# Kernel tuning notes

Measured on AMD Instinct MI355X. Metric: run time of the kernel, lower is better.

The kernel has to match this reference:

```python
import jax, jax.numpy as jnp
import numpy as np

LN_EPS = 1e-6
IGNORE_INDEX = -100

D_MODEL = 768
VOCAB = 32128
B, S = 4, 512


def setup_inputs() -> dict:
    key = jax.random.key(0)
    k1, k2, k3 = jax.random.split(key, 3)
    hidden_states = jax.random.normal(k1, (B, S, D_MODEL), dtype=jnp.float32)
    labels = jax.random.randint(k2, (B, S), 0, VOCAB, dtype=jnp.int64)
    ln_weight = jnp.ones((D_MODEL,), dtype=jnp.float32)
    # nn.Linear(d_model, vocab, bias=False).weight has shape [vocab, d_model]
    lm_head_weight = jax.random.normal(k3, (VOCAB, D_MODEL), dtype=jnp.float32) * (D_MODEL ** -0.5)
    return {
        "hidden_states": hidden_states,
        "labels": labels,
        "ln_weight": ln_weight,
        "lm_head_weight": lm_head_weight,
    }


def t5_layer_norm(x, weight, eps=LN_EPS):
    # T5-style RMSNorm: no mean subtraction, variance in fp32
    variance = jnp.mean(x.astype(jnp.float32) ** 2, axis=-1, keepdims=True)
    x = x * jax.lax.rsqrt(variance + eps)
    return weight * x


def reference(hidden_states, labels, ln_weight, lm_head_weight):
    h = t5_layer_norm(hidden_states, ln_weight)
    # dropout is identity in eval / rate=0
    # lm_head: [B,S,D] @ [V,D]^T -> [B,S,V]
    prediction_scores = jnp.einsum("bsd,vd->bsv", h, lm_head_weight)
    # CrossEntropyLoss(ignore_index=-100), mean over non-ignored tokens
    logits = prediction_scores.reshape(-1, VOCAB)  # [B*S, V]
    flat_labels = labels.reshape(-1)
    valid = flat_labels != IGNORE_INDEX
    safe_labels = jnp.where(valid, flat_labels, 0)
    logp = jax.nn.log_softmax(logits, axis=-1)
    nll = -jnp.take_along_axis(logp, safe_labels[:, None], axis=-1)[:, 0]
    nll = jnp.where(valid, nll, 0.0)
    loss = jnp.sum(nll) / jnp.maximum(jnp.sum(valid.astype(jnp.float32)), 1.0)
    return (loss, prediction_scores)
```

## Files before the change

kernel.cpp:

```cpp
#include <hip/hip_runtime.h>
#include <stdint.h>

#define DM 768
#define VOC 32128
#define NTOK 2048
#define IGN (-100)

typedef __bf16 bf16x8 __attribute__((ext_vector_type(8)));
typedef float f32x4 __attribute__((ext_vector_type(4)));

typedef __attribute__((address_space(1))) void gvoid_t;
typedef __attribute__((address_space(3))) void svoid_t;

__device__ __forceinline__ void gl_lds16(const void* g, void* s) {
  __builtin_amdgcn_global_load_lds((gvoid_t*)g, (svoid_t*)s, 16, 0, 0);
}

__device__ __forceinline__ unsigned short f2bf(float f) {
  unsigned int u = __float_as_uint(f);
  u = (u + 0x7fffu + ((u >> 16) & 1u)) >> 16;
  return (unsigned short)u;
}

__global__ void __launch_bounds__(256) cvt_w_kernel(const float* __restrict__ W,
                                                    unsigned short* __restrict__ Wb) {
  size_t i = ((size_t)blockIdx.x * 256 + threadIdx.x) * 4;
  float4 v = *(const float4*)(W + i);
  ushort4 o;
  o.x = f2bf(v.x); o.y = f2bf(v.y); o.z = f2bf(v.z); o.w = f2bf(v.w);
  *(ushort4*)(Wb + i) = o;
}

__global__ void __launch_bounds__(256) rmsnorm_kernel(const float* __restrict__ x,
                                                      const float* __restrict__ w,
                                                      unsigned short* __restrict__ h) {
  int tok = blockIdx.x;
  const float* xr = x + (size_t)tok * DM;
  int t = threadIdx.x;
  float v0 = xr[t], v1 = xr[t + 256], v2 = xr[t + 512];
  float ss = v0 * v0 + v1 * v1 + v2 * v2;
  for (int off = 32; off; off >>= 1) ss += __shfl_down(ss, off);
  __shared__ float red[4];
  int wv = t >> 6, ln = t & 63;
  if (ln == 0) red[wv] = ss;
  __syncthreads();
  float tot = red[0] + red[1] + red[2] + red[3];
  float inv = rsqrtf(tot * (1.0f / DM) + 1e-6f);
  unsigned short* hr = h + (size_t)tok * DM;
  hr[t]       = f2bf(v0 * inv * w[t]);
  hr[t + 256] = f2bf(v1 * inv * w[t + 256]);
  hr[t + 512] = f2bf(v2 * inv * w[t + 512]);
}

__global__ void __launch_bounds__(256, 2) gemm_kernel(const unsigned short* __restrict__ A,
                                                      const unsigned short* __restrict__ Bw,
                                                      float* __restrict__ C) {
  __shared__ __align__(16) unsigned short As[128 * 32];
  __shared__ __align__(16) unsigned short Bs[128 * 32];

  const int m0 = blockIdx.x * 128;
  const int n0 = blockIdx.y * 128;
  const int tid = threadIdx.x;
  const int wv = tid >> 6, ln = tid & 63;
  const int srow = ln >> 2;
  const int scol = (ln & 3) * 8;

  const unsigned short* aSrc0 = A + (size_t)(m0 + wv * 32 + srow) * DM + scol;
  const unsigned short* aSrc1 = aSrc0 + (size_t)16 * DM;
  const unsigned short* bSrc0 = Bw + (size_t)(n0 + wv * 32 + srow) * DM + scol;
  const unsigned short* bSrc1 = bSrc0 + (size_t)16 * DM;
  unsigned short* aDst0 = &As[(wv * 32) * 32];
  unsigned short* aDst1 = &As[(wv * 32 + 16) * 32];
  unsigned short* bDst0 = &Bs[(wv * 32) * 32];
  unsigned short* bDst1 = &Bs[(wv * 32 + 16) * 32];

  const int quad = ln >> 4, l15 = ln & 15;
  const int wr = (wv >> 1) * 64;
  const int wc = (wv & 1) * 64;

  f32x4 acc[4][4];
#pragma unroll
  for (int i = 0; i < 4; ++i)
#pragma unroll
    for (int j = 0; j < 4; ++j) {
      acc[i][j][0] = 0.f; acc[i][j][1] = 0.f; acc[i][j][2] = 0.f; acc[i][j][3] = 0.f;
    }

  for (int kt = 0; kt < 24; ++kt) {
    const int ko = kt * 32;
    gl_lds16(aSrc0 + ko, aDst0);
    gl_lds16(aSrc1 + ko, aDst1);
    gl_lds16(bSrc0 + ko, bDst0);
    gl_lds16(bSrc1 + ko, bDst1);
    __syncthreads();

    bf16x8 af[4], bfv[4];
#pragma unroll
    for (int i = 0; i < 4; ++i) {
      af[i]  = *(const bf16x8*)(As + (wr + i * 16 + l15) * 32 + quad * 8);
      bfv[i] = *(const bf16x8*)(Bs + (wc + i * 16 + l15) * 32 + quad * 8);
    }
#pragma unroll
    for (int mi = 0; mi < 4; ++mi)
#pragma unroll
      for (int ni = 0; ni < 4; ++ni)
        acc[mi][ni] = __builtin_amdgcn_mfma_f32_16x16x32_bf16(af[mi], bfv[ni], acc[mi][ni], 0, 0, 0);
    __syncthreads();
  }

#pragma unroll
  for (int mi = 0; mi < 4; ++mi) {
#pragma unroll
    for (int r = 0; r < 4; ++r) {
      const int row = m0 + wr + mi * 16 + quad * 4 + r;
      float* cp = C + (size_t)row * VOC + (n0 + wc + l15);
#pragma unroll
      for (int ni = 0; ni < 4; ++ni) cp[ni * 16] = acc[mi][ni][r];
    }
  }
}

__global__ void __launch_bounds__(256) loss_kernel(const float* __restrict__ scores,
                                                   const int* __restrict__ labels,
                                                   float* __restrict__ nll) {
  const int tok = blockIdx.x;
  const float* row = scores + (size_t)tok * VOC;
  float m = -1e30f, s = 0.f;
  for (int j = threadIdx.x; j < VOC; j += 256) {
    float v = row[j];
    float nm = fmaxf(m, v);
    s = s * __expf(m - nm) + __expf(v - nm);
    m = nm;
  }
  for (int off = 32; off; off >>= 1) {
    float m2 = __shfl_down(m, off), s2 = __shfl_down(s, off);
    float nm = fmaxf(m, m2);
    s = s * __expf(m - nm) + s2 * __expf(m2 - nm);
    m = nm;
  }
  __shared__ float ms[4], sh[4];
  int wv = threadIdx.x >> 6, ln = threadIdx.x & 63;
  if (ln == 0) { ms[wv] = m; sh[wv] = s; }
  __syncthreads();
  if (threadIdx.x == 0) {
    float M = ms[0], S = sh[0];
    for (int i = 1; i < 4; ++i) {
      float nm = fmaxf(M, ms[i]);
      S = S * __expf(M - nm) + sh[i] * __expf(ms[i] - nm);
      M = nm;
    }
    int lab = labels[tok];
    float v = 0.f;
    if (lab != IGN) v = (M + logf(S)) - row[lab];
    nll[tok] = v;
  }
}

__global__ void __launch_bounds__(256) reduce_kernel(const float* __restrict__ nll,
                                                     const int* __restrict__ labels,
                                                     float* __restrict__ out) {
  float s = 0.f, c = 0.f;
  for (int i = threadIdx.x; i < NTOK; i += 256) {
    s += nll[i];
    c += (labels[i] != IGN) ? 1.0f : 0.0f;
  }
  for (int off = 32; off; off >>= 1) { s += __shfl_down(s, off); c += __shfl_down(c, off); }
  __shared__ float rs[4], rc[4];
  int wv = threadIdx.x >> 6, ln = threadIdx.x & 63;
  if (ln == 0) { rs[wv] = s; rc[wv] = c; }
  __syncthreads();
  if (threadIdx.x == 0) {
    float S = rs[0] + rs[1] + rs[2] + rs[3];
    float Cc = rc[0] + rc[1] + rc[2] + rc[3];
    out[0] = S / fmaxf(Cc, 1.0f);
  }
}

extern "C" void kernel_launch(void* const* d_in, const int* in_sizes, int n_in,
                              void* d_out, int out_size, void* d_ws, size_t ws_size,
                              hipStream_t stream) {
  const float* hs     = (const float*)d_in[0];
  const int*   labels = (const int*)d_in[1];
  const float* lnw    = (const float*)d_in[2];
  const float* W      = (const float*)d_in[3];

  float* out    = (float*)d_out;
  float* scores = out + 1;

  unsigned short* Wb = (unsigned short*)d_ws;
  unsigned short* Hb = (unsigned short*)((char*)d_ws + (size_t)VOC * DM * 2);
  float* nll         = (float*)((char*)d_ws + (size_t)VOC * DM * 2 + (size_t)NTOK * DM * 2);

  cvt_w_kernel<<<(VOC * DM / 4) / 256, 256, 0, stream>>>(W, Wb);
  rmsnorm_kernel<<<NTOK, 256, 0, stream>>>(hs, lnw, Hb);
  gemm_kernel<<<dim3(NTOK / 128, VOC / 128), 256, 0, stream>>>(Hb, Wb, scores);
  loss_kernel<<<NTOK, 256, 0, stream>>>(scores, labels, nll);
  reduce_kernel<<<1, 256, 0, stream>>>(nll, labels, out);
}
```

Before: 553.5 us.

## Fuse per-tile softmax partials into GEMM epilogue and swizzle LDS layout

The GEMM epilogue now computes a per-row max and sum-exp for each 128-column tile and writes these partials to workspace. A small finalize kernel merges the 251 partials per token, which replaces the full re-read of the 2048x32128 fp32 score matrix. It also XOR-swizzles the LDS column layout to cut bank conflicts on fragment reads, and makes score stores nontemporal. The cost is extra epilogue work, including shuffles and two block syncs, plus more workspace.

Measured after the change: 474.2 us. 1.17x faster.

```diff
diff --git a/kernel.cpp b/kernel.cpp
--- a/kernel.cpp
+++ b/kernel.cpp
@@ -4,6 +4,7 @@
 #define DM 768
 #define VOC 32128
 #define NTOK 2048
+#define NBY (VOC / 128)
 #define IGN (-100)
 
 typedef __bf16 bf16x8 __attribute__((ext_vector_type(8)));
@@ -54,16 +55,19 @@
 
 __global__ void __launch_bounds__(256, 2) gemm_kernel(const unsigned short* __restrict__ A,
                                                       const unsigned short* __restrict__ Bw,
-                                                      float* __restrict__ C) {
+                                                      float* __restrict__ C,
+                                                      float* __restrict__ Pm,
+                                                      float* __restrict__ Ps) {
   __shared__ __align__(16) unsigned short As[128 * 32];
   __shared__ __align__(16) unsigned short Bs[128 * 32];
 
   const int m0 = blockIdx.x * 128;
   const int n0 = blockIdx.y * 128;
+  const int by = blockIdx.y;
   const int tid = threadIdx.x;
   const int wv = tid >> 6, ln = tid & 63;
   const int srow = ln >> 2;
-  const int scol = (ln & 3) * 8;
+  const int scol = ((ln & 3) ^ ((srow >> 1) & 3)) * 8;
 
   const unsigned short* aSrc0 = A + (size_t)(m0 + wv * 32 + srow) * DM + scol;
   const unsigned short* aSrc1 = aSrc0 + (size_t)16 * DM;
@@ -75,6 +79,7 @@
   unsigned short* bDst1 = &Bs[(wv * 32 + 16) * 32];
 
   const int quad = ln >> 4, l15 = ln & 15;
+  const int slot = (quad ^ ((l15 >> 1) & 3)) * 8;
   const int wr = (wv >> 1) * 64;
   const int wc = (wv & 1) * 64;
 
@@ -97,8 +102,8 @@
     bf16x8 af[4], bfv[4];
 #pragma unroll
     for (int i = 0; i < 4; ++i) {
-      af[i]  = *(const bf16x8*)(As + (wr + i * 16 + l15) * 32 + quad * 8);
-      bfv[i] = *(const bf16x8*)(Bs + (wc + i * 16 + l15) * 32 + quad * 8);
+      af[i]  = *(const bf16x8*)(As + (wr + i * 16 + l15) * 32 + slot);
+      bfv[i] = *(const bf16x8*)(Bs + (wc + i * 16 + l15) * 32 + slot);
     }
 #pragma unroll
     for (int mi = 0; mi < 4; ++mi)
@@ -115,21 +120,61 @@
       const int row = m0 + wr + mi * 16 + quad * 4 + r;
       float* cp = C + (size_t)row * VOC + (n0 + wc + l15);
 #pragma unroll
-      for (int ni = 0; ni < 4; ++ni) cp[ni * 16] = acc[mi][ni][r];
-    }
-  }
-}
-
-__global__ void __launch_bounds__(256) loss_kernel(const float* __restrict__ scores,
-                                                   const int* __restrict__ labels,
-                                                   float* __restrict__ nll) {
+      for (int ni = 0; ni < 4; ++ni)
+        __builtin_nontemporal_store(acc[mi][ni][r], cp + ni * 16);
+    }
+  }
+
+  float* pmL = (float*)As;
+  float* psL = (float*)Bs;
+  float rm[4][4], rs[4][4];
+#pragma unroll
+  for (int mi = 0; mi < 4; ++mi) {
+#pragma unroll
+    for (int r = 0; r < 4; ++r) {
+      float m = fmaxf(fmaxf(acc[mi][0][r], acc[mi][1][r]),
+                      fmaxf(acc[mi][2][r], acc[mi][3][r]));
+#pragma unroll
+      for (int off = 1; off < 16; off <<= 1) m = fmaxf(m, __shfl_xor(m, off));
+      float s = __expf(acc[mi][0][r] - m) + __expf(acc[mi][1][r] - m) +
+                __expf(acc[mi][2][r] - m) + __expf(acc[mi][3][r] - m);
+#pragma unroll
+      for (int off = 1; off < 16; off <<= 1) s += __shfl_xor(s, off);
+      rm[mi][r] = m; rs[mi][r] = s;
+    }
+  }
+  __syncthreads();
+  if (l15 == 0) {
+#pragma unroll
+    for (int mi = 0; mi < 4; ++mi)
+#pragma unroll
+      for (int r = 0; r < 4; ++r) {
+        int row = wr + mi * 16 + quad * 4 + r;
+        pmL[(wv & 1) * 128 + row] = rm[mi][r];
+        psL[(wv & 1) * 128 + row] = rs[mi][r];
+      }
+  }
+  __syncthreads();
+  if (tid < 128) {
+    float ma = pmL[tid], mb = pmL[128 + tid];
+    float nm = fmaxf(ma, mb);
+    float S = psL[tid] * __expf(ma - nm) + psL[128 + tid] * __expf(mb - nm);
+    Pm[(size_t)by * NTOK + m0 + tid] = nm;
+    Ps[(size_t)by * NTOK + m0 + tid] = S;
+  }
+}
+
+__global__ void __launch_bounds__(256) loss_finalize_kernel(const float* __restrict__ Pm,
+                                                            const float* __restrict__ Ps,
+                                                            const float* __restrict__ scores,
+                                                            const int* __restrict__ labels,
+                                                            float* __restrict__ nll) {
   const int tok = blockIdx.x;
-  const float* row = scores + (size_t)tok * VOC;
   float m = -1e30f, s = 0.f;
-  for (int j = threadIdx.x; j < VOC; j += 256) {
-    float v = row[j];
-    float nm = fmaxf(m, v);
-    s = s * __expf(m - nm) + __expf(v - nm);
+  for (int j = threadIdx.x; j < NBY; j += 256) {
+    float m2 = Pm[(size_t)j * NTOK + tok], s2 = Ps[(size_t)j * NTOK + tok];
+    float nm = fmaxf(m, m2);
+    s = s * __expf(m - nm) + s2 * __expf(m2 - nm);
     m = nm;
   }
   for (int off = 32; off; off >>= 1) {
@@ -151,7 +196,7 @@
     }
     int lab = labels[tok];
     float v = 0.f;
-    if (lab != IGN) v = (M + logf(S)) - row[lab];
+    if (lab != IGN) v = (M + logf(S)) - scores[(size_t)tok * VOC + lab];
     nll[tok] = v;
   }
 }
@@ -187,13 +232,16 @@
   float* out    = (float*)d_out;
   float* scores = out + 1;
 
-  unsigned short* Wb = (unsigned short*)d_ws;
-  unsigned short* Hb = (unsigned short*)((char*)d_ws + (size_t)VOC * DM * 2);
-  float* nll         = (float*)((char*)d_ws + (size_t)VOC * DM * 2 + (size_t)NTOK * DM * 2);
+  char* ws = (char*)d_ws;
+  unsigned short* Wb = (unsigned short*)ws;                 ws += (size_t)VOC * DM * 2;
+  unsigned short* Hb = (unsigned short*)ws;                 ws += (size_t)NTOK * DM * 2;
+  float* Pm          = (float*)ws;                          ws += (size_t)NBY * NTOK * 4;
+  float* Ps          = (float*)ws;                          ws += (size_t)NBY * NTOK * 4;
+  float* nll         = (float*)ws;
 
   cvt_w_kernel<<<(VOC * DM / 4) / 256, 256, 0, stream>>>(W, Wb);
   rmsnorm_kernel<<<NTOK, 256, 0, stream>>>(hs, lnw, Hb);
-  gemm_kernel<<<dim3(NTOK / 128, VOC / 128), 256, 0, stream>>>(Hb, Wb, scores);
-  loss_kernel<<<NTOK, 256, 0, stream>>>(scores, labels, nll);
+  gemm_kernel<<<dim3(NTOK / 128, VOC / 128), 256, 0, stream>>>(Hb, Wb, scores, Pm, Ps);
+  loss_finalize_kernel<<<NTOK, 256, 0, stream>>>(Pm, Ps, scores, labels, nll);
   reduce_kernel<<<1, 256, 0, stream>>>(nll, labels, out);
 }
```
